# Kernel optimization log

Measured on AMD Instinct MI355X. Metric: run time of the kernel, lower is better.

The kernel has to match this reference:

```python
import jax, jax.numpy as jnp
import numpy as np

C_IN = 1024
C_INTER = 512
EPS = 1e-5
STD = 0.01


def _conv1x1(x, w, b):
    # x: [B,C,H,W], w: [O,C] (1x1 conv kernel squeezed), b: [O]
    return jnp.einsum('bchw,oc->bohw', x, w) + b[None, :, None, None]


def setup_inputs() -> dict:
    key = jax.random.key(0)
    ks = jax.random.split(key, 12)
    def w(k, o, i):
        return jax.random.normal(k, (o, i), jnp.float32) * STD
    def b(k, o):
        return jax.random.normal(k, (o,), jnp.float32) * STD
    return {
        'x': jax.random.normal(ks[0], (8, C_IN, 64, 64), jnp.float32),
        'theta_w': w(ks[1], C_INTER, C_IN), 'theta_b': b(ks[2], C_INTER),
        'phi_w': w(ks[3], C_INTER, C_IN), 'phi_b': b(ks[4], C_INTER),
        'g_w': w(ks[5], C_INTER, C_IN), 'g_b': b(ks[6], C_INTER),
        'wz_w': w(ks[7], C_IN, C_INTER), 'wz_b': b(ks[8], C_IN),
        'bn_gamma': jax.random.normal(ks[9], (C_IN,), jnp.float32) * 0.1,
        'bn_beta': jax.random.normal(ks[10], (C_IN,), jnp.float32) * 0.1,
    }


def reference(x, theta_w, theta_b, phi_w, phi_b, g_w, g_b, wz_w, wz_b, bn_gamma, bn_beta):
    B, C, H, W = x.shape
    # theta on full-res input: [B, Ci, H*W]
    theta = _conv1x1(x, theta_w, theta_b).reshape(B, C_INTER, H * W)
    # 2x2 stride-2 max pool for phi/g path
    xp = jax.lax.reduce_window(x, -jnp.inf, jax.lax.max,
                               (1, 1, 2, 2), (1, 1, 2, 2), 'VALID')
    Hp, Wp = xp.shape[2], xp.shape[3]
    phi = _conv1x1(xp, phi_w, phi_b).reshape(B, C_INTER, Hp * Wp)
    g = _conv1x1(xp, g_w, g_b).reshape(B, C_INTER, Hp * Wp)
    # attention: [B, H*W, Hp*Wp], scaled softmax
    attn = jnp.einsum('bcn,bcm->bnm', theta, phi) * (C_INTER ** -0.5)
    attn = jax.nn.softmax(attn, axis=-1)
    # aggregate: [B, Ci, H*W]
    y = jnp.einsum('bcm,bnm->bcn', g, attn).reshape(B, C_INTER, H, W)
    z = _conv1x1(y, wz_w, wz_b)
    # BatchNorm2d (training-mode batch stats, biased var)
    mean = z.mean(axis=(0, 2, 3), keepdims=True)
    var = jnp.mean((z - mean) ** 2, axis=(0, 2, 3), keepdims=True)
    z = (z - mean) * jax.lax.rsqrt(var + EPS)
    z = z * bn_gamma[None, :, None, None] + bn_beta[None, :, None, None]
    return x + z
```

## Files before the change

### kernel.cpp

```cpp
#include <hip/hip_runtime.h>

typedef unsigned short u16;
typedef unsigned int u32;
typedef __attribute__((ext_vector_type(8))) short bf16x8;
typedef __attribute__((ext_vector_type(4))) float f32x4;

__device__ __forceinline__ u16 f2bf(float f) {
  u32 u = __builtin_bit_cast(u32, f);
  u = u + 0x7FFFu + ((u >> 16) & 1u);
  return (u16)(u >> 16);
}
__device__ __forceinline__ float bf2f(u16 s) {
  return __builtin_bit_cast(float, (u32)s << 16);
}

__device__ __forceinline__ void gload_lds16(const u16* g, u16* l) {
  __builtin_amdgcn_global_load_lds(
      (const __attribute__((address_space(1))) u32*)g,
      (__attribute__((address_space(3))) u32*)l, 16, 0, 0);
}

__global__ __launch_bounds__(256) void k_cvt(const float* __restrict__ s,
                                             u16* __restrict__ d) {
  int i = (blockIdx.x * 256 + threadIdx.x) * 4;
  float4 v = *(const float4*)(s + i);
  u32 lo = (u32)f2bf(v.x) | ((u32)f2bf(v.y) << 16);
  u32 hi = (u32)f2bf(v.z) | ((u32)f2bf(v.w) << 16);
  uint2 o; o.x = lo; o.y = hi;
  *(uint2*)(d + i) = o;
}

__global__ __launch_bounds__(256) void k_transpose_pool(
    const float* __restrict__ x, u16* __restrict__ xT, u16* __restrict__ xpT) {
  __shared__ u16 lds[128 * 64];
  const int t = threadIdx.x;
  const int c0 = blockIdx.x * 64;
  const int by = blockIdx.y;
  const int b = blockIdx.z;

  {
    const int nf = (t & 31) * 4;
    const int swz = 8 * (t & 7);
    const float* xb =
        x + ((size_t)(b * 1024 + c0 + (t >> 5)) * 4096) + by * 128 + nf;
#pragma unroll
    for (int u = 0; u < 8; ++u) {
      const int c_l = (t >> 5) + 8 * u;
      float4 v = *(const float4*)(xb + (size_t)(8 * u) * 4096);
      const int col = c_l ^ swz;
      lds[(nf + 0) * 64 + col] = f2bf(v.x);
      lds[(nf + 1) * 64 + col] = f2bf(v.y);
      lds[(nf + 2) * 64 + col] = f2bf(v.z);
      lds[(nf + 3) * 64 + col] = f2bf(v.w);
    }
  }
  __syncthreads();
  {
#pragma unroll
    for (int v = 0; v < 4; ++v) {
      const int idx = t + 256 * v;
      const int n_l = idx >> 3;
      const int cb = (idx & 7) * 8;
      const int col = cb ^ (8 * ((n_l >> 2) & 7));
      bf16x8 d = *(const bf16x8*)&lds[n_l * 64 + col];
      *(bf16x8*)&xT[((size_t)b * 4096 + by * 128 + n_l) * 1024 + c0 + cb] = d;
    }
  }
  {
    const int m_w = t >> 3;
    const int cb = (t & 7) * 8;
    const int na = 2 * m_w, nb = na + 1, nc = na + 64, nd = na + 65;
    bf16x8 va = *(const bf16x8*)&lds[na * 64 + (cb ^ (8 * ((na >> 2) & 7)))];
    bf16x8 vb = *(const bf16x8*)&lds[nb * 64 + (cb ^ (8 * ((nb >> 2) & 7)))];
    bf16x8 vc = *(const bf16x8*)&lds[nc * 64 + (cb ^ (8 * ((nc >> 2) & 7)))];
    bf16x8 vd = *(const bf16x8*)&lds[nd * 64 + (cb ^ (8 * ((nd >> 2) & 7)))];
    bf16x8 o;
#pragma unroll
    for (int j = 0; j < 8; ++j) {
      float m = fmaxf(fmaxf(bf2f((u16)va[j]), bf2f((u16)vb[j])),
                      fmaxf(bf2f((u16)vc[j]), bf2f((u16)vd[j])));
      o[j] = (short)f2bf(m);
    }
    *(bf16x8*)&xpT[((size_t)b * 1024 + by * 32 + m_w) * 1024 + c0 + cb] = o;
  }
}

template <int BIAS_MODE>
__global__ __launch_bounds__(256, 2) void gemm_nt(
    const u16* __restrict__ A, long aBS, const u16* __restrict__ Bm, long bBS,
    u16* __restrict__ Cm, long cBS, const float* __restrict__ bias, int N,
    int K, float scale) {
  __shared__ u16 Alds[2][128 * 32];
  __shared__ u16 Blds[2][128 * 32];
  const int t = threadIdx.x;
  const int b = blockIdx.z;
  const int bm = blockIdx.y, bn = blockIdx.x;
  const u16* Ab = A + (size_t)b * aBS + (size_t)bm * 128 * K;
  const u16* Bb = Bm + (size_t)b * bBS + (size_t)bn * 128 * K;

  const int lane = t & 63;
  const int w = t >> 6;
  const int wrow = w >> 1, wcol = w & 1;
  const int lr = lane & 15;
  const int kg = lane >> 4;

  f32x4 acc[4][4] = {};

  const int e0 = t * 8;
  const int r0 = e0 >> 5;
  const int k0i = e0 & 31;
  const int steps = K >> 5;

#define STAGE(buf, ks)                                                   \
  do {                                                                   \
    const int kb = (ks) * 32;                                            \
    gload_lds16(Ab + (size_t)r0 * K + kb + k0i, &Alds[buf][e0]);         \
    gload_lds16(Ab + (size_t)(r0 + 64) * K + kb + k0i,                   \
                &Alds[buf][e0 + 2048]);                                  \
    gload_lds16(Bb + (size_t)r0 * K + kb + k0i, &Blds[buf][e0]);         \
    gload_lds16(Bb + (size_t)(r0 + 64) * K + kb + k0i,                   \
                &Blds[buf][e0 + 2048]);                                  \
  } while (0)

  STAGE(0, 0);
  for (int ks = 0; ks < steps; ++ks) {
    const int cur = ks & 1;
    __syncthreads();
    if (ks + 1 < steps) STAGE(cur ^ 1, ks + 1);
    bf16x8 af[4], bfr[4];
#pragma unroll
    for (int i = 0; i < 4; ++i) {
      af[i] =
          *(const bf16x8*)&Alds[cur][(wrow * 64 + i * 16 + lr) * 32 + kg * 8];
      bfr[i] =
          *(const bf16x8*)&Blds[cur][(wcol * 64 + i * 16 + lr) * 32 + kg * 8];
    }
#pragma unroll
    for (int i = 0; i < 4; ++i)
#pragma unroll
      for (int j = 0; j < 4; ++j)
        acc[i][j] = __builtin_amdgcn_mfma_f32_16x16x32_bf16(af[i], bfr[j],
                                                            acc[i][j], 0, 0, 0);
  }
#undef STAGE

  u16* Cb = Cm + (size_t)b * cBS;
#pragma unroll
  for (int i = 0; i < 4; ++i) {
#pragma unroll
    for (int j = 0; j < 4; ++j) {
      int row0 = bm * 128 + wrow * 64 + i * 16 + kg * 4;
      int col = bn * 128 + wcol * 64 + j * 16 + lr;
      float bj = (BIAS_MODE == 2) ? bias[col] : 0.f;
#pragma unroll
      for (int r = 0; r < 4; ++r) {
        float v = acc[i][j][r] * scale;
        if (BIAS_MODE == 1) v += bias[row0 + r];
        if (BIAS_MODE == 2) v += bj;
        Cb[(size_t)(row0 + r) * N + col] = f2bf(v);
      }
    }
  }
}

__global__ __launch_bounds__(256) void k_softmax(u16* __restrict__ S) {
  const int t = threadIdx.x;
  const int lane = t & 63;
  const size_t row = (size_t)blockIdx.x * 4 + (t >> 6);
  u16* p = S + row * 1024 + lane * 16;
  uint4 d0 = *(const uint4*)p;
  uint4 d1 = *(const uint4*)(p + 8);
  u32 u[8] = {d0.x, d0.y, d0.z, d0.w, d1.x, d1.y, d1.z, d1.w};
  float v[16];
#pragma unroll
  for (int i = 0; i < 8; ++i) {
    v[2 * i] = bf2f((u16)(u[i] & 0xffff));
    v[2 * i + 1] = bf2f((u16)(u[i] >> 16));
  }
  float m = v[0];
#pragma unroll
  for (int i = 1; i < 16; ++i) m = fmaxf(m, v[i]);
  for (int o = 32; o > 0; o >>= 1) m = fmaxf(m, __shfl_xor(m, o));
  const float LOG2E = 1.44269504088896f;
  float s = 0.f;
#pragma unroll
  for (int i = 0; i < 16; ++i) {
    v[i] = exp2f((v[i] - m) * LOG2E);
    s += v[i];
  }
  for (int o = 32; o > 0; o >>= 1) s += __shfl_xor(s, o);
  float inv = 1.0f / s;
#pragma unroll
  for (int i = 0; i < 8; ++i)
    u[i] = (u32)f2bf(v[2 * i] * inv) | ((u32)f2bf(v[2 * i + 1] * inv) << 16);
  uint4 o0; o0.x = u[0]; o0.y = u[1]; o0.z = u[2]; o0.w = u[3];
  uint4 o1; o1.x = u[4]; o1.y = u[5]; o1.z = u[6]; o1.w = u[7];
  *(uint4*)p = o0;
  *(uint4*)(p + 8) = o1;
}

__global__ __launch_bounds__(256) void k_stats(const u16* __restrict__ z,
                                               float2* __restrict__ stats) {
  const int o = blockIdx.x;
  const int t = threadIdx.x;
  float s = 0.f, q = 0.f;
  for (int b = 0; b < 8; ++b) {
    const u16* p = z + ((size_t)b * 1024 + o) * 4096;
    for (int i = t * 4; i < 4096; i += 1024) {
      uint2 d = *(const uint2*)(p + i);
      float a0 = bf2f((u16)(d.x & 0xffff)), a1 = bf2f((u16)(d.x >> 16));
      float a2 = bf2f((u16)(d.y & 0xffff)), a3 = bf2f((u16)(d.y >> 16));
      s += a0 + a1 + a2 + a3;
      q += a0 * a0 + a1 * a1 + a2 * a2 + a3 * a3;
    }
  }
  for (int o2 = 32; o2 > 0; o2 >>= 1) {
    s += __shfl_xor(s, o2);
    q += __shfl_xor(q, o2);
  }
  __shared__ float2 red[4];
  if ((t & 63) == 0) red[t >> 6] = make_float2(s, q);
  __syncthreads();
  if (t == 0) {
    float S_ = 0.f, Q_ = 0.f;
    for (int i = 0; i < 4; ++i) { S_ += red[i].x; Q_ += red[i].y; }
    stats[o] = make_float2(S_, Q_);
  }
}

__global__ __launch_bounds__(256) void k_apply(
    const float* __restrict__ x, const u16* __restrict__ z,
    const float2* __restrict__ stats, const float* __restrict__ gamma,
    const float* __restrict__ beta, float* __restrict__ out) {
  size_t i4 = (size_t)blockIdx.x * 256 + threadIdx.x;
  size_t e = i4 * 4;
  int c = (int)((e >> 12) & 1023);
  float2 st = stats[c];
  const float cnt = 1.0f / 32768.0f;
  float mean = st.x * cnt;
  float var = st.y * cnt - mean * mean;
  float g = rsqrtf(var + 1e-5f) * gamma[c];
  float sh = beta[c] - mean * g;
  float4 xv = *(const float4*)(x + e);
  uint2 zd = *(const uint2*)(z + e);
  float z0 = bf2f((u16)(zd.x & 0xffff)), z1 = bf2f((u16)(zd.x >> 16));
  float z2 = bf2f((u16)(zd.y & 0xffff)), z3 = bf2f((u16)(zd.y >> 16));
  float4 ov;
  ov.x = xv.x + z0 * g + sh;
  ov.y = xv.y + z1 * g + sh;
  ov.z = xv.z + z2 * g + sh;
  ov.w = xv.w + z3 * g + sh;
  *(float4*)(out + e) = ov;
}

extern "C" void kernel_launch(void* const* d_in, const int* in_sizes, int n_in,
                              void* d_out, int out_size, void* d_ws,
                              size_t ws_size, hipStream_t stream) {
  const float* x = (const float*)d_in[0];
  const float* theta_w = (const float*)d_in[1];
  const float* theta_b = (const float*)d_in[2];
  const float* phi_w = (const float*)d_in[3];
  const float* phi_b = (const float*)d_in[4];
  const float* g_w = (const float*)d_in[5];
  const float* g_b = (const float*)d_in[6];
  const float* wz_w = (const float*)d_in[7];
  const float* wz_b = (const float*)d_in[8];
  const float* gamma = (const float*)d_in[9];
  const float* beta = (const float*)d_in[10];
  float* out = (float*)d_out;

  char* w = (char*)d_ws;
  const size_t MiB = (size_t)1 << 20;
  u16* WT = (u16*)(w + 0 * MiB);
  u16* WP = (u16*)(w + 1 * MiB);
  u16* WG = (u16*)(w + 2 * MiB);
  u16* WZ = (u16*)(w + 3 * MiB);
  u16* XT = (u16*)(w + 4 * MiB);
  u16* XPT = (u16*)(w + 68 * MiB);
  u16* THETA = (u16*)(w + 84 * MiB);
  u16* PHI = (u16*)(w + 116 * MiB);
  u16* G = (u16*)(w + 124 * MiB);
  u16* S = XT;
  u16* YT = (u16*)(w + 132 * MiB);
  u16* Z = S;
  float2* stats = (float2*)(w + 164 * MiB);

  k_cvt<<<512, 256, 0, stream>>>(theta_w, WT);
  k_cvt<<<512, 256, 0, stream>>>(phi_w, WP);
  k_cvt<<<512, 256, 0, stream>>>(g_w, WG);
  k_cvt<<<512, 256, 0, stream>>>(wz_w, WZ);
  k_transpose_pool<<<dim3(16, 32, 8), 256, 0, stream>>>(x, XT, XPT);
  gemm_nt<2><<<dim3(4, 32, 8), 256, 0, stream>>>(
      XT, (long)4096 * 1024, WT, 0, THETA, (long)4096 * 512, theta_b, 512,
      1024, 1.0f);
  gemm_nt<2><<<dim3(4, 8, 8), 256, 0, stream>>>(
      XPT, (long)1024 * 1024, WP, 0, PHI, (long)1024 * 512, phi_b, 512, 1024,
      1.0f);
  gemm_nt<1><<<dim3(8, 4, 8), 256, 0, stream>>>(
      WG, 0, XPT, (long)1024 * 1024, G, (long)512 * 1024, g_b, 1024, 1024,
      1.0f);
  gemm_nt<0><<<dim3(8, 32, 8), 256, 0, stream>>>(
      THETA, (long)4096 * 512, PHI, (long)1024 * 512, S, (long)4096 * 1024,
      nullptr, 1024, 512, 0.04419417382415922f);
  k_softmax<<<8192, 256, 0, stream>>>(S);
  gemm_nt<0><<<dim3(4, 32, 8), 256, 0, stream>>>(
      S, (long)4096 * 1024, G, (long)512 * 1024, YT, (long)4096 * 512, nullptr,
      512, 1024, 1.0f);
  gemm_nt<1><<<dim3(32, 8, 8), 256, 0, stream>>>(
      WZ, 0, YT, (long)4096 * 512, Z, (long)1024 * 4096, wz_b, 4096, 512,
      1.0f);
  k_stats<<<1024, 256, 0, stream>>>(Z, stats);
  k_apply<<<32768, 256, 0, stream>>>(x, Z, stats, gamma, beta, out);

  (void)in_sizes; (void)n_in; (void)out_size; (void)ws_size;
}
```

Before: 579.5 us.

## Replace GEMM with 256x256-tile, 8-wave kernel with swizzled LDS and interleaved staging

```diff
diff --git a/kernel.cpp b/kernel.cpp
--- a/kernel.cpp
+++ b/kernel.cpp
@@ -86,81 +86,140 @@
 }
 
 template <int BIAS_MODE>
-__global__ __launch_bounds__(256, 2) void gemm_nt(
+__global__ __launch_bounds__(512) void gemm256(
     const u16* __restrict__ A, long aBS, const u16* __restrict__ Bm, long bBS,
     u16* __restrict__ Cm, long cBS, const float* __restrict__ bias, int N,
     int K, float scale) {
-  __shared__ u16 Alds[2][128 * 32];
-  __shared__ u16 Blds[2][128 * 32];
+  __shared__ u16 ALDS[2][16384];
+  __shared__ u16 BLDS[2][16384];
   const int t = threadIdx.x;
-  const int b = blockIdx.z;
-  const int bm = blockIdx.y, bn = blockIdx.x;
-  const u16* Ab = A + (size_t)b * aBS + (size_t)bm * 128 * K;
-  const u16* Bb = Bm + (size_t)b * bBS + (size_t)bn * 128 * K;
+  u32 gx = gridDim.x, gy = gridDim.y;
+  u32 nwg = gx * gy * gridDim.z;
+  u32 wg = blockIdx.x + gx * (blockIdx.y + gy * blockIdx.z);
+  u32 swz = (wg & 7) * (nwg >> 3) + (wg >> 3);
+  const int bn = swz % gx;
+  u32 tmp = swz / gx;
+  const int bm = tmp % gy;
+  const int b = tmp / gy;
+
+  const u16* Agb = A + (size_t)b * aBS + (size_t)bm * 256 * K;
+  const u16* Bgb = Bm + (size_t)b * bBS + (size_t)bn * 256 * K;
 
   const int lane = t & 63;
-  const int w = t >> 6;
-  const int wrow = w >> 1, wcol = w & 1;
+  const int wid = t >> 6;
+  const int wr = wid >> 2;
+  const int wc = wid & 3;
   const int lr = lane & 15;
-  const int kg = lane >> 4;
-
-  f32x4 acc[4][4] = {};
-
-  const int e0 = t * 8;
-  const int r0 = e0 >> 5;
-  const int k0i = e0 & 31;
-  const int steps = K >> 5;
-
-#define STAGE(buf, ks)                                                   \
-  do {                                                                   \
-    const int kb = (ks) * 32;                                            \
-    gload_lds16(Ab + (size_t)r0 * K + kb + k0i, &Alds[buf][e0]);         \
-    gload_lds16(Ab + (size_t)(r0 + 64) * K + kb + k0i,                   \
-                &Alds[buf][e0 + 2048]);                                  \
-    gload_lds16(Bb + (size_t)r0 * K + kb + k0i, &Blds[buf][e0]);         \
-    gload_lds16(Bb + (size_t)(r0 + 64) * K + kb + k0i,                   \
-                &Blds[buf][e0 + 2048]);                                  \
-  } while (0)
-
-  STAGE(0, 0);
-  for (int ks = 0; ks < steps; ++ks) {
-    const int cur = ks & 1;
-    __syncthreads();
-    if (ks + 1 < steps) STAGE(cur ^ 1, ks + 1);
-    bf16x8 af[4], bfr[4];
-#pragma unroll
-    for (int i = 0; i < 4; ++i) {
-      af[i] =
-          *(const bf16x8*)&Alds[cur][(wrow * 64 + i * 16 + lr) * 32 + kg * 8];
-      bfr[i] =
-          *(const bf16x8*)&Blds[cur][(wcol * 64 + i * 16 + lr) * 32 + kg * 8];
-    }
-#pragma unroll
-    for (int i = 0; i < 4; ++i)
-#pragma unroll
-      for (int j = 0; j < 4; ++j)
-        acc[i][j] = __builtin_amdgcn_mfma_f32_16x16x32_bf16(af[i], bfr[j],
-                                                            acc[i][j], 0, 0, 0);
-  }
-#undef STAGE
+  const int kg = (lane >> 4) & 3;
+  const int T = K >> 6;
+
+  f32x4 acc[8][4] = {};
+
+#define STAGE_G(LDSARR, GB, h, ktn)                                          \
+  if ((ktn) < T) {                                                           \
+    {                                                                        \
+      const int r = t >> 3;                                                  \
+      gload_lds16(GB + (size_t)((h)*128 + r) * K + (size_t)(ktn)*64 +        \
+                      (((t & 7) ^ (r & 7)) * 8),                             \
+                  &LDSARR[(ktn) & 1][(h)*8192 + t * 8]);                     \
+    }                                                                        \
+    {                                                                        \
+      const int idx = 512 + t;                                               \
+      const int r = idx >> 3;                                                \
+      gload_lds16(GB + (size_t)((h)*128 + r) * K + (size_t)(ktn)*64 +        \
+                      (((t & 7) ^ (r & 7)) * 8),                             \
+                  &LDSARR[(ktn) & 1][(h)*8192 + idx * 8]);                   \
+    }                                                                        \
+  }
+#define STAGE_A(h, ktn) STAGE_G(ALDS, Agb, h, ktn)
+#define STAGE_B(h, ktn) STAGE_G(BLDS, Bgb, h, ktn)
+
+#define LDA4(mh, kk)                                                         \
+  _Pragma("unroll") for (int m2 = 0; m2 < 4; ++m2) {                         \
+    const int row = wr * 128 + ((mh)*4 + m2) * 16 + lr;                      \
+    aF[m2] = *(const bf16x8*)&ALDS[cb][row * 64 +                            \
+                                       ((((kk)*4 + kg) ^ (lr & 7)) * 8)];    \
+  }
+#define LDB4(kk)                                                             \
+  _Pragma("unroll") for (int n = 0; n < 4; ++n) {                            \
+    const int row = wc * 64 + n * 16 + lr;                                   \
+    bF[n] = *(const bf16x8*)&BLDS[cb][row * 64 +                             \
+                                      ((((kk)*4 + kg) ^ (lr & 7)) * 8)];     \
+  }
+#define MFMA16(M0)                                                           \
+  __builtin_amdgcn_s_setprio(1);                                             \
+  _Pragma("unroll") for (int n = 0; n < 4; ++n) {                            \
+    acc[(M0) + 0][n] = __builtin_amdgcn_mfma_f32_16x16x32_bf16(              \
+        aF[0], bF[n], acc[(M0) + 0][n], 0, 0, 0);                            \
+    acc[(M0) + 1][n] = __builtin_amdgcn_mfma_f32_16x16x32_bf16(              \
+        aF[1], bF[n], acc[(M0) + 1][n], 0, 0, 0);                            \
+    acc[(M0) + 2][n] = __builtin_amdgcn_mfma_f32_16x16x32_bf16(              \
+        aF[2], bF[n], acc[(M0) + 2][n], 0, 0, 0);                            \
+    acc[(M0) + 3][n] = __builtin_amdgcn_mfma_f32_16x16x32_bf16(              \
+        aF[3], bF[n], acc[(M0) + 3][n], 0, 0, 0);                            \
+  }                                                                          \
+  __builtin_amdgcn_s_setprio(0);
+#define CFENCE asm volatile("" ::: "memory")
+
+  STAGE_B(0, 0);
+  STAGE_B(1, 0);
+  STAGE_A(0, 0);
+  STAGE_A(1, 0);
+  STAGE_B(0, 1);
+
+  for (int kt = 0; kt < T; ++kt) {
+    const int cb = kt & 1;
+    bf16x8 aF[4], bF[4];
+    asm volatile("s_waitcnt vmcnt(2)" ::: "memory");
+    __builtin_amdgcn_s_barrier();
+    STAGE_B(1, kt + 1);
+    LDB4(0);
+    LDA4(0, 0);
+    MFMA16(0);
+    CFENCE;
+    __builtin_amdgcn_s_barrier();
+    STAGE_A(0, kt + 1);
+    LDA4(1, 0);
+    MFMA16(4);
+    CFENCE;
+    __builtin_amdgcn_s_barrier();
+    STAGE_A(1, kt + 1);
+    LDB4(1);
+    LDA4(0, 1);
+    MFMA16(0);
+    CFENCE;
+    __builtin_amdgcn_s_barrier();
+    STAGE_B(0, kt + 2);
+    LDA4(1, 1);
+    MFMA16(4);
+    CFENCE;
+    __builtin_amdgcn_s_barrier();
+  }
 
   u16* Cb = Cm + (size_t)b * cBS;
 #pragma unroll
-  for (int i = 0; i < 4; ++i) {
-#pragma unroll
-    for (int j = 0; j < 4; ++j) {
-      int row0 = bm * 128 + wrow * 64 + i * 16 + kg * 4;
-      int col = bn * 128 + wcol * 64 + j * 16 + lr;
+  for (int m = 0; m < 8; ++m) {
+    const int row0 = bm * 256 + wr * 128 + m * 16 + kg * 4;
+#pragma unroll
+    for (int n = 0; n < 4; ++n) {
+      const int col = bn * 256 + wc * 64 + n * 16 + lr;
       float bj = (BIAS_MODE == 2) ? bias[col] : 0.f;
 #pragma unroll
       for (int r = 0; r < 4; ++r) {
-        float v = acc[i][j][r] * scale;
+        float v = acc[m][n][r] * scale;
         if (BIAS_MODE == 1) v += bias[row0 + r];
         if (BIAS_MODE == 2) v += bj;
         Cb[(size_t)(row0 + r) * N + col] = f2bf(v);
       }
     }
   }
+#undef STAGE_G
+#undef STAGE_A
+#undef STAGE_B
+#undef LDA4
+#undef LDB4
+#undef MFMA16
+#undef CFENCE
 }
 
 __global__ __launch_bounds__(256) void k_softmax(u16* __restrict__ S) {
@@ -290,23 +349,21 @@
   k_cvt<<<512, 256, 0, stream>>>(g_w, WG);
   k_cvt<<<512, 256, 0, stream>>>(wz_w, WZ);
   k_transpose_pool<<<dim3(16, 32, 8), 256, 0, stream>>>(x, XT, XPT);
-  gemm_nt<2><<<dim3(4, 32, 8), 256, 0, stream>>>(
-      XT, (long)4096 * 1024, WT, 0, THETA, (long)4096 * 512, theta_b, 512,
-      1024, 1.0f);
-  gemm_nt<2><<<dim3(4, 8, 8), 256, 0, stream>>>(
-      XPT, (long)1024 * 1024, WP, 0, PHI, (long)1024 * 512, phi_b, 512, 1024,
-      1.0f);
-  gemm_nt<1><<<dim3(8, 4, 8), 256, 0, stream>>>(
+  gemm256<2><<<dim3(2, 128, 1), 512, 0, stream>>>(
+      XT, 0, WT, 0, THETA, 0, theta_b, 512, 1024, 1.0f);
+  gemm256<2><<<dim3(2, 32, 1), 512, 0, stream>>>(
+      XPT, 0, WP, 0, PHI, 0, phi_b, 512, 1024, 1.0f);
+  gemm256<1><<<dim3(4, 2, 8), 512, 0, stream>>>(
       WG, 0, XPT, (long)1024 * 1024, G, (long)512 * 1024, g_b, 1024, 1024,
       1.0f);
-  gemm_nt<0><<<dim3(8, 32, 8), 256, 0, stream>>>(
+  gemm256<0><<<dim3(4, 16, 8), 512, 0, stream>>>(
       THETA, (long)4096 * 512, PHI, (long)1024 * 512, S, (long)4096 * 1024,
       nullptr, 1024, 512, 0.04419417382415922f);
   k_softmax<<<8192, 256, 0, stream>>>(S);
-  gemm_nt<0><<<dim3(4, 32, 8), 256, 0, stream>>>(
+  gemm256<0><<<dim3(2, 16, 8), 512, 0, stream>>>(
       S, (long)4096 * 1024, G, (long)512 * 1024, YT, (long)4096 * 512, nullptr,
       512, 1024, 1.0f);
-  gemm_nt<1><<<dim3(32, 8, 8), 256, 0, stream>>>(
+  gemm256<1><<<dim3(16, 4, 8), 512, 0, stream>>>(
       WZ, 0, YT, (long)4096 * 512, Z, (long)1024 * 4096, wz_b, 4096, 512,
       1.0f);
   k_stats<<<1024, 256, 0, stream>>>(Z, stats);
```

New measurement: 631.6 us. 9.0% more time.
